# Kernel tuning notes

Measured on AMD Instinct MI355X. Metric: run time of the kernel, lower is better.

Reference implementation:

```python
import jax, jax.numpy as jnp
import numpy as np

DIM = 128
HEADS = 4
DIM_HEAD = 32
HIDDEN = HEADS * DIM_HEAD  # 128
EPS = 1e-5


def setup_inputs() -> dict:
    key = jax.random.key(0)
    ks = jax.random.split(key, 5)
    x = jax.random.normal(ks[0], (32, DIM, 64, 64), dtype=jnp.float32)
    # 1x1 convs are channel matmuls
    Wqkv = jax.random.normal(ks[1], (HIDDEN * 3, DIM), dtype=jnp.float32) * (1.0 / np.sqrt(DIM))
    Wout = jax.random.normal(ks[2], (DIM, HIDDEN), dtype=jnp.float32) * (1.0 / np.sqrt(HIDDEN))
    bout = jnp.zeros((DIM,), dtype=jnp.float32)
    ln_w = jnp.ones((DIM,), dtype=jnp.float32)
    ln_b = jnp.zeros((DIM,), dtype=jnp.float32)
    return {"x": x, "Wqkv": Wqkv, "Wout": Wout, "bout": bout, "ln_w": ln_w, "ln_b": ln_b}


def reference(x, Wqkv, Wout, bout, ln_w, ln_b):
    b, c, h, w = x.shape
    n = h * w
    xf = x.reshape(b, c, n)  # b c n
    qkv = jnp.einsum('oc,bcn->bon', Wqkv, xf)  # b (3*hidden) n
    q, k, v = jnp.split(qkv, 3, axis=1)
    # b (h d) n -> b h d n
    q = q.reshape(b, HEADS, DIM_HEAD, n)
    k = k.reshape(b, HEADS, DIM_HEAD, n)
    v = v.reshape(b, HEADS, DIM_HEAD, n)
    q = jax.nn.softmax(q, axis=-2)  # over feature dim d
    k = jax.nn.softmax(k, axis=-1)  # over spatial dim n
    context = jnp.einsum('bhdn,bhen->bhde', k, v)
    out = jnp.einsum('bhde,bhdn->bhen', context, q)  # b h e n
    out = out.reshape(b, HIDDEN, n)
    out = jnp.einsum('oc,bcn->bon', Wout, out) + bout[None, :, None]
    out = out.reshape(b, DIM, h, w)
    # LayerNorm2d over channel dim, biased variance
    mean = jnp.mean(out, axis=1, keepdims=True)
    var = jnp.var(out, axis=1, keepdims=True)
    out = (out - mean) / jnp.sqrt(var + EPS) * ln_w[None, :, None, None] + ln_b[None, :, None, None]
    return out
```

## Files before the change

### kernel.cpp

```cpp
#include <hip/hip_runtime.h>
#include <stdint.h>


constexpr int B_   = 32;
constexpr int C_   = 128;
constexpr int N_   = 4096;
constexpr int O3_  = 384;
constexpr int NSUB = 8;
constexpr int TPB_ = 8;

using short8  = __attribute__((ext_vector_type(8))) short;
using short4v = __attribute__((ext_vector_type(4))) short;
using float4v = __attribute__((ext_vector_type(4))) float;

__device__ __forceinline__ unsigned short bf16_rne(float f) {
    union { float f; uint32_t u; } v; v.f = f;
    uint32_t u = v.u;
    u += 0x7FFFu + ((u >> 16) & 1u);
    return (unsigned short)(u >> 16);
}
__device__ __forceinline__ float bf2f(unsigned short h) {
    union { uint32_t u; float f; } v; v.u = ((uint32_t)h) << 16; return v.f;
}

constexpr size_t OFF_WQ   = 0;
constexpr size_t OFF_WO   = 98304;
constexpr size_t OFF_SP   = 131072;
constexpr size_t OFF_CTXP = 262144;
constexpr size_t OFF_WBIG = 4456448;
constexpr size_t OFF_QSM  = 5505024;

__global__ __launch_bounds__(256) void k0_prep(const float* __restrict__ Wqkv,
                                               const float* __restrict__ Wout,
                                               unsigned short* __restrict__ wq,
                                               unsigned short* __restrict__ wo) {
    int t = blockIdx.x * 256 + threadIdx.x;
    if (t < O3_ * C_) wq[t] = bf16_rne(Wqkv[t]);
    if (t < C_ * C_)  wo[t] = bf16_rne(Wout[t]);
}

__global__ __launch_bounds__(1024) void k1_qkv(const float* __restrict__ x,
                                               const unsigned short* __restrict__ wq,
                                               unsigned short* __restrict__ qsm,
                                               float* __restrict__ ctx_part,
                                               float* __restrict__ S_part) {
    __shared__ __align__(16) unsigned short xs0[64 * 136];
    __shared__ __align__(16) unsigned short xs1[64 * 136];
    __shared__ __align__(16) unsigned short ek[128 * 72];
    __shared__ __align__(16) unsigned short vsh[128 * 72];

    const int b    = blockIdx.y;
    const int tblk = blockIdx.x;
    const int tid  = threadIdx.x;

    const int lane = tid & 63;
    const int wv   = tid >> 6;
    const int l15  = lane & 15;
    const int quad = lane >> 4;

    const float4v zero = {0.f, 0.f, 0.f, 0.f};

    short8 wfa[8];
    if (wv < 12) {
        const unsigned short* wqp = wq + (wv * 32 + l15) * C_ + quad * 8;
        #pragma unroll
        for (int kk = 0; kk < 4; kk++) {
            wfa[kk]     = *(const short8*)(wqp + kk * 32);
            wfa[4 + kk] = *(const short8*)(wqp + 16 * C_ + kk * 32);
        }
    }

    const int sid = tid & 255;
    const int snl = sid & 63;
    const int scg = sid >> 6;
    const float* xbase = x + ((size_t)b * C_ + (size_t)scg * 32) * N_ + snl;
    float xv[32];
    auto load_x = [&](int s) {
        const float* xp = xbase + (tblk * NSUB + s) * 64;
        #pragma unroll
        for (int i = 0; i < 32; i++) xv[i] = xp[(size_t)i * N_];
    };
    auto store_x = [&](unsigned short* xs) {
        unsigned short* dst = &xs[snl * 136 + scg * 32];
        #pragma unroll
        for (int ii = 0; ii < 4; ii++) {
            short8 v8;
            #pragma unroll
            for (int j = 0; j < 8; j++) v8[j] = (short)bf16_rne(xv[ii * 8 + j]);
            *(short8*)(dst + ii * 8) = v8;
        }
    };

    if (wv >= 12) { load_x(0); store_x(xs0); }
    unsigned short* xs_cur = xs0;
    unsigned short* xs_nxt = xs1;

    float4v cacc = zero;
    float s_acc  = 0.f;
    const int ch  = wv >> 2;
    const int cdt = (wv >> 1) & 1;
    const int cet = wv & 1;

    for (int s = 0; s < NSUB; s++) {
        const int ns = (tblk * NSUB + s) * 64;
        __syncthreads();

        if (wv < 12) {
            #pragma unroll
            for (int ct = 0; ct < 4; ct++) {
                short8 bfx[4];
                #pragma unroll
                for (int kk = 0; kk < 4; kk++)
                    bfx[kk] = *(const short8*)&xs_cur[(ct * 16 + l15) * 136 + kk * 32 + quad * 8];
                float4v acc0 = zero, acc1 = zero;
                #pragma unroll
                for (int kk = 0; kk < 4; kk++) {
                    acc0 = __builtin_amdgcn_mfma_f32_16x16x32_bf16(wfa[kk],     bfx[kk], acc0, 0, 0, 0);
                    acc1 = __builtin_amdgcn_mfma_f32_16x16x32_bf16(wfa[4 + kk], bfx[kk], acc1, 0, 0, 0);
                }
                const int ncol = ct * 16 + l15;
                if (wv < 4) {
                    float e0[4], e1[4], z = 0.f;
                    #pragma unroll
                    for (int r = 0; r < 4; r++) {
                        e0[r] = __expf(acc0[r]); e1[r] = __expf(acc1[r]);
                        z += e0[r] + e1[r];
                    }
                    z += __shfl_xor(z, 16, 64);
                    z += __shfl_xor(z, 32, 64);
                    const float iz = 1.0f / z;
                    unsigned short* qp = qsm + ((size_t)b * N_ + ns + ncol) * C_ + wv * 32 + quad * 4;
                    short4v s0, s1;
                    #pragma unroll
                    for (int r = 0; r < 4; r++) {
                        s0[r] = (short)bf16_rne(e0[r] * iz);
                        s1[r] = (short)bf16_rne(e1[r] * iz);
                    }
                    *(short4v*)qp = s0;
                    *(short4v*)(qp + 16) = s1;
                } else if (wv < 8) {
                    const int row0 = (wv - 4) * 32 + quad * 4;
                    #pragma unroll
                    for (int r = 0; r < 4; r++) {
                        ek[(row0 + r) * 72 + ncol]      = bf16_rne(__expf(acc0[r]));
                        ek[(row0 + 16 + r) * 72 + ncol] = bf16_rne(__expf(acc1[r]));
                    }
                } else {
                    const int row0 = (wv - 8) * 32 + quad * 4;
                    #pragma unroll
                    for (int r = 0; r < 4; r++) {
                        vsh[(row0 + r) * 72 + ncol]      = bf16_rne(acc0[r]);
                        vsh[(row0 + 16 + r) * 72 + ncol] = bf16_rne(acc1[r]);
                    }
                }
            }
        } else {
            if (s + 1 < NSUB) { load_x(s + 1); store_x(xs_nxt); }
        }
        __syncthreads();

        {
            const unsigned short* ap = &ek[(ch * 32 + cdt * 16 + l15) * 72 + quad * 8];
            const unsigned short* bp = &vsh[(ch * 32 + cet * 16 + l15) * 72 + quad * 8];
            #pragma unroll
            for (int kk = 0; kk < 2; kk++) {
                short8 a  = *(const short8*)(ap + kk * 32);
                short8 bb = *(const short8*)(bp + kk * 32);
                cacc = __builtin_amdgcn_mfma_f32_16x16x32_bf16(a, bb, cacc, 0, 0, 0);
            }
        }
        {
            const unsigned short* ep = &ek[(tid >> 3) * 72 + (tid & 7) * 8];
            short8 e0 = *(const short8*)ep;
            float ss = 0.f;
            #pragma unroll
            for (int j = 0; j < 8; j++) ss += bf2f((unsigned short)e0[j]);
            s_acc += ss;
        }
        { unsigned short* t = xs_cur; xs_cur = xs_nxt; xs_nxt = t; }
    }

    {
        float* cp = ctx_part + ((size_t)(b * TPB_ + tblk) << 12)
                  + ((ch * 32 + cdt * 16 + quad * 4) * 32 + cet * 16 + l15);
        #pragma unroll
        for (int r = 0; r < 4; r++) cp[r * 32] = cacc[r];
    }
    {
        float ss = s_acc;
        ss += __shfl_xor(ss, 1, 64);
        ss += __shfl_xor(ss, 2, 64);
        ss += __shfl_xor(ss, 4, 64);
        if ((tid & 7) == 0)
            S_part[(size_t)(b * TPB_ + tblk) * 128 + (tid >> 3)] = ss;
    }
}

__global__ __launch_bounds__(512) void k2_reduce(const float* __restrict__ ctx_part,
                                                 const float* __restrict__ S_part,
                                                 const unsigned short* __restrict__ wo,
                                                 unsigned short* __restrict__ wbig) {
    __shared__ float Sinv[128];
    __shared__ __align__(16) unsigned short ctxb[128 * 40];
    const int b   = blockIdx.x;
    const int tid = threadIdx.x;

    if (tid < 128) {
        float s = 0.f;
        #pragma unroll
        for (int t = 0; t < TPB_; t++)
            s += S_part[(size_t)(b * TPB_ + t) * 128 + tid];
        Sinv[tid] = 1.0f / s;
    }
    __syncthreads();

    #pragma unroll
    for (int i = 0; i < 8; i++) {
        const int ei = i * 512 + tid;
        float v = 0.f;
        #pragma unroll
        for (int t = 0; t < TPB_; t++)
            v += ctx_part[((size_t)(b * TPB_ + t) << 12) + ei];
        ctxb[(ei >> 5) * 40 + (ei & 31)] = bf16_rne(v * Sinv[ei >> 5]);
    }
    __syncthreads();

    const int lane = tid & 63, wv = tid >> 6, l15 = lane & 15, quad = lane >> 4;
    const float4v zero = {0.f, 0.f, 0.f, 0.f};
    unsigned short* wb = wbig + (size_t)b * (C_ * C_);
    #pragma unroll
    for (int ht = 0; ht < 8; ht++) {
        const int h_ = ht >> 1;
        short8 a  = *(const short8*)(wo + (wv * 16 + l15) * C_ + h_ * 32 + quad * 8);
        short8 bb = *(const short8*)&ctxb[(h_ * 32 + (ht & 1) * 16 + l15) * 40 + quad * 8];
        float4v c4 = __builtin_amdgcn_mfma_f32_16x16x32_bf16(a, bb, zero, 0, 0, 0);
        #pragma unroll
        for (int r = 0; r < 4; r++)
            wb[(wv * 16 + quad * 4 + r) * C_ + ht * 16 + l15] = bf16_rne(c4[r]);
    }
}

__global__ __launch_bounds__(256) void k3_out(const unsigned short* __restrict__ qsm,
                                              const unsigned short* __restrict__ wbig,
                                              const float* __restrict__ bout,
                                              const float* __restrict__ lnw,
                                              const float* __restrict__ lnb,
                                              float* __restrict__ out) {
    const int b   = blockIdx.y;
    const int n0  = blockIdx.x * 64;
    const int tid = threadIdx.x;

    const int lane = tid & 63, wv = tid >> 6, l15 = lane & 15, quad = lane >> 4;
    const int nl = wv * 16 + l15;
    const size_t n = (size_t)n0 + nl;

    const float4v zero = {0.f, 0.f, 0.f, 0.f};

    short8 bq[4];
    #pragma unroll
    for (int kk = 0; kk < 4; kk++)
        bq[kk] = *(const short8*)(qsm + ((size_t)b * N_ + n) * C_ + kk * 32 + quad * 8);

    const unsigned short* wbp = wbig + (size_t)b * (C_ * C_);
    float4v acc[8];
    #pragma unroll
    for (int ot = 0; ot < 8; ot++) {
        const unsigned short* wp = wbp + (ot * 16 + l15) * C_ + quad * 8;
        short8 w0 = *(const short8*)(wp);
        short8 w1 = *(const short8*)(wp + 32);
        short8 w2 = *(const short8*)(wp + 64);
        short8 w3 = *(const short8*)(wp + 96);
        float4v a = zero;
        a = __builtin_amdgcn_mfma_f32_16x16x32_bf16(w0, bq[0], a, 0, 0, 0);
        a = __builtin_amdgcn_mfma_f32_16x16x32_bf16(w1, bq[1], a, 0, 0, 0);
        a = __builtin_amdgcn_mfma_f32_16x16x32_bf16(w2, bq[2], a, 0, 0, 0);
        a = __builtin_amdgcn_mfma_f32_16x16x32_bf16(w3, bq[3], a, 0, 0, 0);
        acc[ot] = a;
    }

    float sum = 0.f, sq = 0.f;
    #pragma unroll
    for (int ot = 0; ot < 8; ot++) {
        #pragma unroll
        for (int r = 0; r < 4; r++) {
            const int o = ot * 16 + quad * 4 + r;
            const float y = acc[ot][r] + bout[o];
            acc[ot][r] = y;
            sum += y; sq += y * y;
        }
    }
    sum += __shfl_xor(sum, 16, 64);
    sum += __shfl_xor(sum, 32, 64);
    sq  += __shfl_xor(sq, 16, 64);
    sq  += __shfl_xor(sq, 32, 64);
    const float mean = sum * (1.0f / 128.0f);
    const float var  = sq * (1.0f / 128.0f) - mean * mean;
    const float rstd = rsqrtf(var + 1e-5f);

    #pragma unroll
    for (int ot = 0; ot < 8; ot++) {
        #pragma unroll
        for (int r = 0; r < 4; r++) {
            const int o = ot * 16 + quad * 4 + r;
            out[((size_t)b * C_ + o) * N_ + n] = (acc[ot][r] - mean) * rstd * lnw[o] + lnb[o];
        }
    }
}

extern "C" void kernel_launch(void* const* d_in, const int* in_sizes, int n_in,
                              void* d_out, int out_size, void* d_ws, size_t ws_size,
                              hipStream_t stream) {
    const float* x    = (const float*)d_in[0];
    const float* Wqkv = (const float*)d_in[1];
    const float* Wout = (const float*)d_in[2];
    const float* bout = (const float*)d_in[3];
    const float* lnw  = (const float*)d_in[4];
    const float* lnb  = (const float*)d_in[5];
    float* out = (float*)d_out;

    char* ws = (char*)d_ws;
    unsigned short* wq   = (unsigned short*)(ws + OFF_WQ);
    unsigned short* wo   = (unsigned short*)(ws + OFF_WO);
    float* S_part        = (float*)(ws + OFF_SP);
    float* ctx_part      = (float*)(ws + OFF_CTXP);
    unsigned short* wbig = (unsigned short*)(ws + OFF_WBIG);
    unsigned short* qsm  = (unsigned short*)(ws + OFF_QSM);

    k0_prep<<<192, 256, 0, stream>>>(Wqkv, Wout, wq, wo);
    k1_qkv<<<dim3(TPB_, B_), 1024, 0, stream>>>(x, wq, qsm, ctx_part, S_part);
    k2_reduce<<<B_, 512, 0, stream>>>(ctx_part, S_part, wo, wbig);
    k3_out<<<dim3(N_ / 64, B_), 256, 0, stream>>>(qsm, wbig, bout, lnw, lnb, out);
}
```

Measured before the change: 177.7 us.

## Split context reduction across more blocks and stage folded weights in LDS

The per-batch context reduction is split into a wider kernel (256 blocks) that writes normalized bf16 context, followed by a small fold kernel that writes the per-batch folded output weight in an MFMA-fragment-ordered layout. The output kernel now processes 128 positions per 512-thread block and loads the whole folded weight into LDS once with coalesced loads, instead of each wave reading scattered weight rows from global memory. This trades an extra kernel launch and a 32KB LDS footprint per block for better parallelism in the reduction and less redundant global weight traffic.

Measured after the change: 159.9 us. -10.0%, faster.

```diff
diff --git a/kernel.cpp b/kernel.cpp
--- a/kernel.cpp
+++ b/kernel.cpp
@@ -27,8 +27,9 @@
 constexpr size_t OFF_WO   = 98304;
 constexpr size_t OFF_SP   = 131072;
 constexpr size_t OFF_CTXP = 262144;
-constexpr size_t OFF_WBIG = 4456448;
-constexpr size_t OFF_QSM  = 5505024;
+constexpr size_t OFF_CTXN = 4456448;
+constexpr size_t OFF_WBIG = 4718592;
+constexpr size_t OFF_QSM  = 5767168;
 
 __global__ __launch_bounds__(256) void k0_prep(const float* __restrict__ Wqkv,
                                                const float* __restrict__ Wout,
@@ -196,58 +197,72 @@
     }
 }
 
-__global__ __launch_bounds__(512) void k2_reduce(const float* __restrict__ ctx_part,
-                                                 const float* __restrict__ S_part,
-                                                 const unsigned short* __restrict__ wo,
-                                                 unsigned short* __restrict__ wbig) {
-    __shared__ float Sinv[128];
-    __shared__ __align__(16) unsigned short ctxb[128 * 40];
+__global__ __launch_bounds__(256) void k2a_reduce(const float* __restrict__ ctx_part,
+                                                  const float* __restrict__ S_part,
+                                                  unsigned short* __restrict__ ctxn) {
+    __shared__ float Sinv[16];
+    const int b     = blockIdx.x >> 3;
+    const int chunk = blockIdx.x & 7;
+    const int tid   = threadIdx.x;
+    if (tid < 16) {
+        const int hd = chunk * 16 + tid;
+        float s = 0.f;
+        #pragma unroll
+        for (int t = 0; t < TPB_; t++)
+            s += S_part[(size_t)(b * TPB_ + t) * 128 + hd];
+        Sinv[tid] = 1.0f / s;
+    }
+    __syncthreads();
+    #pragma unroll
+    for (int j = 0; j < 2; j++) {
+        const int ei = chunk * 512 + j * 256 + tid;
+        float v = 0.f;
+        #pragma unroll
+        for (int t = 0; t < TPB_; t++)
+            v += ctx_part[((size_t)(b * TPB_ + t) << 12) + ei];
+        ctxn[(size_t)b * 4096 + ei] = bf16_rne(v * Sinv[(ei >> 5) - chunk * 16]);
+    }
+}
+
+__global__ __launch_bounds__(512) void k2b_fold(const unsigned short* __restrict__ ctxn,
+                                                const unsigned short* __restrict__ wo,
+                                                unsigned short* __restrict__ wbig) {
     const int b   = blockIdx.x;
     const int tid = threadIdx.x;
-
-    if (tid < 128) {
-        float s = 0.f;
-        #pragma unroll
-        for (int t = 0; t < TPB_; t++)
-            s += S_part[(size_t)(b * TPB_ + t) * 128 + tid];
-        Sinv[tid] = 1.0f / s;
-    }
-    __syncthreads();
-
-    #pragma unroll
-    for (int i = 0; i < 8; i++) {
-        const int ei = i * 512 + tid;
-        float v = 0.f;
-        #pragma unroll
-        for (int t = 0; t < TPB_; t++)
-            v += ctx_part[((size_t)(b * TPB_ + t) << 12) + ei];
-        ctxb[(ei >> 5) * 40 + (ei & 31)] = bf16_rne(v * Sinv[ei >> 5]);
-    }
-    __syncthreads();
-
     const int lane = tid & 63, wv = tid >> 6, l15 = lane & 15, quad = lane >> 4;
     const float4v zero = {0.f, 0.f, 0.f, 0.f};
+
+    short8 a4[4], b8[8];
+    #pragma unroll
+    for (int h = 0; h < 4; h++)
+        a4[h] = *(const short8*)(wo + (wv * 16 + l15) * C_ + h * 32 + quad * 8);
+    #pragma unroll
+    for (int ht = 0; ht < 8; ht++)
+        b8[ht] = *(const short8*)(ctxn + (size_t)b * 4096
+                                  + ((ht >> 1) * 32 + (ht & 1) * 16 + l15) * 32 + quad * 8);
+
     unsigned short* wb = wbig + (size_t)b * (C_ * C_);
     #pragma unroll
     for (int ht = 0; ht < 8; ht++) {
-        const int h_ = ht >> 1;
-        short8 a  = *(const short8*)(wo + (wv * 16 + l15) * C_ + h_ * 32 + quad * 8);
-        short8 bb = *(const short8*)&ctxb[(h_ * 32 + (ht & 1) * 16 + l15) * 40 + quad * 8];
-        float4v c4 = __builtin_amdgcn_mfma_f32_16x16x32_bf16(a, bb, zero, 0, 0, 0);
+        float4v c4 = __builtin_amdgcn_mfma_f32_16x16x32_bf16(a4[ht >> 1], b8[ht], zero, 0, 0, 0);
+        const int c     = wv * 4 + (ht >> 1);
+        const int quadp = (ht & 1) * 2 + (l15 >> 3);
         #pragma unroll
         for (int r = 0; r < 4; r++)
-            wb[(wv * 16 + quad * 4 + r) * C_ + ht * 16 + l15] = bf16_rne(c4[r]);
-    }
-}
-
-__global__ __launch_bounds__(256) void k3_out(const unsigned short* __restrict__ qsm,
+            wb[((c * 64 + quadp * 16 + quad * 4 + r) << 3) + (l15 & 7)] = bf16_rne(c4[r]);
+    }
+}
+
+__global__ __launch_bounds__(512) void k3_out(const unsigned short* __restrict__ qsm,
                                               const unsigned short* __restrict__ wbig,
                                               const float* __restrict__ bout,
                                               const float* __restrict__ lnw,
                                               const float* __restrict__ lnb,
                                               float* __restrict__ out) {
+    __shared__ __align__(16) unsigned short wls[16384];
+
     const int b   = blockIdx.y;
-    const int n0  = blockIdx.x * 64;
+    const int n0  = blockIdx.x * 128;
     const int tid = threadIdx.x;
 
     const int lane = tid & 63, wv = tid >> 6, l15 = lane & 15, quad = lane >> 4;
@@ -256,25 +271,30 @@
 
     const float4v zero = {0.f, 0.f, 0.f, 0.f};
 
+    short8 st[4];
+    {
+        const short8* src = (const short8*)(wbig + (size_t)b * (C_ * C_));
+        #pragma unroll
+        for (int i = 0; i < 4; i++) st[i] = src[i * 512 + tid];
+    }
     short8 bq[4];
     #pragma unroll
     for (int kk = 0; kk < 4; kk++)
         bq[kk] = *(const short8*)(qsm + ((size_t)b * N_ + n) * C_ + kk * 32 + quad * 8);
-
-    const unsigned short* wbp = wbig + (size_t)b * (C_ * C_);
+    #pragma unroll
+    for (int i = 0; i < 4; i++)
+        *(short8*)&wls[(i * 512 + tid) * 8] = st[i];
+    __syncthreads();
+
     float4v acc[8];
     #pragma unroll
     for (int ot = 0; ot < 8; ot++) {
-        const unsigned short* wp = wbp + (ot * 16 + l15) * C_ + quad * 8;
-        short8 w0 = *(const short8*)(wp);
-        short8 w1 = *(const short8*)(wp + 32);
-        short8 w2 = *(const short8*)(wp + 64);
-        short8 w3 = *(const short8*)(wp + 96);
         float4v a = zero;
-        a = __builtin_amdgcn_mfma_f32_16x16x32_bf16(w0, bq[0], a, 0, 0, 0);
-        a = __builtin_amdgcn_mfma_f32_16x16x32_bf16(w1, bq[1], a, 0, 0, 0);
-        a = __builtin_amdgcn_mfma_f32_16x16x32_bf16(w2, bq[2], a, 0, 0, 0);
-        a = __builtin_amdgcn_mfma_f32_16x16x32_bf16(w3, bq[3], a, 0, 0, 0);
+        #pragma unroll
+        for (int kk = 0; kk < 4; kk++) {
+            short8 w = *(const short8*)&wls[(((ot * 4 + kk) * 64 + lane)) * 8];
+            a = __builtin_amdgcn_mfma_f32_16x16x32_bf16(w, bq[kk], a, 0, 0, 0);
+        }
         acc[ot] = a;
     }
 
@@ -323,11 +343,13 @@
     unsigned short* wo   = (unsigned short*)(ws + OFF_WO);
     float* S_part        = (float*)(ws + OFF_SP);
     float* ctx_part      = (float*)(ws + OFF_CTXP);
+    unsigned short* ctxn = (unsigned short*)(ws + OFF_CTXN);
     unsigned short* wbig = (unsigned short*)(ws + OFF_WBIG);
     unsigned short* qsm  = (unsigned short*)(ws + OFF_QSM);
 
     k0_prep<<<192, 256, 0, stream>>>(Wqkv, Wout, wq, wo);
     k1_qkv<<<dim3(TPB_, B_), 1024, 0, stream>>>(x, wq, qsm, ctx_part, S_part);
-    k2_reduce<<<B_, 512, 0, stream>>>(ctx_part, S_part, wo, wbig);
-    k3_out<<<dim3(N_ / 64, B_), 256, 0, stream>>>(qsm, wbig, bout, lnw, lnb, out);
-}
+    k2a_reduce<<<B_ * 8, 256, 0, stream>>>(ctx_part, S_part, ctxn);
+    k2b_fold<<<B_, 512, 0, stream>>>(ctxn, wo, wbig);
+    k3_out<<<dim3(N_ / 128, B_), 512, 0, stream>>>(qsm, wbig, bout, lnw, lnb, out);
+}
```
